# Optimization experiments

Hardware: AMD Instinct MI355X
Metric: run time of the kernel (lower is better)

The kernel has to match this reference:

```python
import jax, jax.numpy as jnp
import numpy as np

D_IN = 1024
D_OUT = 1024
N_HEADS = 16
HEAD_DIM = D_OUT // N_HEADS

def setup_inputs() -> dict:
    key = jax.random.key(0)
    ks = jax.random.split(key, 6)
    s = 0.02
    x = jax.random.normal(ks[0], (2, 2048, D_IN), dtype=jnp.float32)
    Wq = jax.random.normal(ks[1], (D_IN, D_OUT), dtype=jnp.float32) * s
    Wk = jax.random.normal(ks[2], (D_IN, D_OUT), dtype=jnp.float32) * s
    Wv = jax.random.normal(ks[3], (D_IN, D_OUT), dtype=jnp.float32) * s
    Wo = jax.random.normal(ks[4], (D_OUT, D_OUT), dtype=jnp.float32) * s
    bo = jnp.zeros((D_OUT,), dtype=jnp.float32)
    return {"x": x, "Wq": Wq, "Wk": Wk, "Wv": Wv, "Wo": Wo, "bo": bo}

def reference(x, Wq, Wk, Wv, Wo, bo):
    b, t, _ = x.shape
    # project and split heads: [b, h, t, d]
    def split_heads(y):
        return y.reshape(b, t, N_HEADS, HEAD_DIM).transpose(0, 2, 1, 3)
    q = split_heads(x @ Wq)
    k = split_heads(x @ Wk)
    v = split_heads(x @ Wv)
    # NOTE: original code applies NO 1/sqrt(head_dim) scaling
    scores = jnp.einsum('bhqd,bhkd->bhqk', q, k)
    causal = jnp.tril(jnp.ones((t, t), dtype=bool))  # keep lower triangle
    scores = jnp.where(causal, scores, -jnp.inf)
    attn = jax.nn.softmax(scores, axis=-1)
    ctx = jnp.einsum('bhqk,bhkd->bhqd', attn, v)
    ctx = ctx.transpose(0, 2, 1, 3).reshape(b, t, D_OUT)
    return ctx @ Wo + bo
```

## Files before the change

### kernel.cpp

```cpp
#include <hip/hip_runtime.h>

typedef unsigned short u16;
typedef unsigned int   u32;
typedef __bf16 bf16x2 __attribute__((ext_vector_type(2)));
typedef __bf16 bf16x8 __attribute__((ext_vector_type(8)));
typedef float  f32x4  __attribute__((ext_vector_type(4)));
typedef float  f32x16 __attribute__((ext_vector_type(16)));
typedef u32    u32x4  __attribute__((ext_vector_type(4)));

#define LOG2E 1.4426950408889634f

__device__ __forceinline__ u16 f2bf(float f) {
  union { float f; u32 u; } v; v.f = f;
  u32 r = v.u + 0x7fffu + ((v.u >> 16) & 1u);
  return (u16)(r >> 16);
}

__device__ __forceinline__ u32 pack2(float lo, float hi) {
  bf16x2 p = { (__bf16)lo, (__bf16)hi };
  return __builtin_bit_cast(u32, p);
}

#define GLOAD_LDS16(g, s) __builtin_amdgcn_global_load_lds( \
    (const __attribute__((address_space(1))) void*)(g),     \
    (__attribute__((address_space(3))) void*)(s), 16, 0, 0)


__global__ void k_convert(const float* __restrict__ in, u16* __restrict__ out) {
  int i = (blockIdx.x * 256 + threadIdx.x) * 8;
  float4 a = *(const float4*)(in + i);
  float4 b = *(const float4*)(in + i + 4);
  u16 o[8] = { f2bf(a.x), f2bf(a.y), f2bf(a.z), f2bf(a.w),
               f2bf(b.x), f2bf(b.y), f2bf(b.z), f2bf(b.w) };
  *(uint4*)(out + i) = *(const uint4*)o;
}

__global__ void k_transpose_w4(const float* __restrict__ Wq, const float* __restrict__ Wk,
                               const float* __restrict__ Wv, const float* __restrict__ Wo,
                               u16* __restrict__ WqkvT, u16* __restrict__ WoT) {
  const int z = blockIdx.z;
  const float* W = (z == 0) ? Wq : (z == 1) ? Wk : (z == 2) ? Wv : Wo;
  u16* WT = (z < 3) ? (WqkvT + ((size_t)z << 20)) : WoT;
  __shared__ float tile[64][65];
  const int t = threadIdx.x;
  const int n0 = blockIdx.x * 64, k0 = blockIdx.y * 64;
  const int r = t >> 4, c4 = (t & 15) * 4;
  #pragma unroll
  for (int rr = 0; rr < 64; rr += 16) {
    float4 v = *(const float4*)(W + (size_t)(k0 + r + rr) * 1024 + n0 + c4);
    tile[r + rr][c4]     = v.x; tile[r + rr][c4 + 1] = v.y;
    tile[r + rr][c4 + 2] = v.z; tile[r + rr][c4 + 3] = v.w;
  }
  __syncthreads();
  #pragma unroll
  for (int rr = 0; rr < 64; rr += 16) {
    u16 o[4] = { f2bf(tile[c4][r + rr]),     f2bf(tile[c4 + 1][r + rr]),
                 f2bf(tile[c4 + 2][r + rr]), f2bf(tile[c4 + 3][r + rr]) };
    *(ushort4*)(WT + (size_t)(n0 + r + rr) * 1024 + k0 + c4) = *(const ushort4*)o;
  }
}


template<int MODE>
__global__ __launch_bounds__(256) void k_gemm_bt(
    const u16* __restrict__ A, const u16* __restrict__ BT,
    void* __restrict__ Cv, const float* __restrict__ bias,
    int M, int N, int K) {
  __shared__ u16 lA[2][128 * 32];
  __shared__ u16 lB[2][128 * 32];
  const int t = threadIdx.x;
  const int l = t & 63, w = t >> 6;
  const int bM = blockIdx.y * 128, bN = blockIdx.x * 128;
  const int wr = w >> 1, wc = w & 1;
  const int NT = K >> 5;

  f32x4 acc[4][4] = {};

  const int fA  = w * 512 + l * 8;
  const int r0  = fA >> 5;
  const int kc0 = fA & 31;

  auto stage = [&](int buf, int kt) {
    const u16* ga = A  + (size_t)(bM + r0) * K + kt * 32 + kc0;
    const u16* gb = BT + (size_t)(bN + r0) * K + kt * 32 + kc0;
    GLOAD_LDS16(ga, &lA[buf][w * 512]);
    GLOAD_LDS16(gb, &lB[buf][w * 512]);
    GLOAD_LDS16(ga + (size_t)64 * K, &lA[buf][2048 + w * 512]);
    GLOAD_LDS16(gb + (size_t)64 * K, &lB[buf][2048 + w * 512]);
  };

  stage(0, 0);
  __syncthreads();
  int buf = 0;
  for (int kt = 0; kt < NT; ++kt) {
    if (kt + 1 < NT) stage(buf ^ 1, kt + 1);
    bf16x8 af[4], bfr[4];
    #pragma unroll
    for (int m = 0; m < 4; ++m)
      af[m] = *(const bf16x8*)&lA[buf][(wr * 64 + m * 16 + (l & 15)) * 32 + (l >> 4) * 8];
    #pragma unroll
    for (int n = 0; n < 4; ++n)
      bfr[n] = *(const bf16x8*)&lB[buf][(wc * 64 + n * 16 + (l & 15)) * 32 + (l >> 4) * 8];
    #pragma unroll
    for (int m = 0; m < 4; ++m)
      #pragma unroll
      for (int n = 0; n < 4; ++n)
        acc[m][n] = __builtin_amdgcn_mfma_f32_16x16x32_bf16(af[m], bfr[n], acc[m][n], 0, 0, 0);
    __syncthreads();
    buf ^= 1;
  }

  #pragma unroll
  for (int m = 0; m < 4; ++m) {
    #pragma unroll
    for (int n = 0; n < 4; ++n) {
      const int row = bM + wr * 64 + m * 16 + (l >> 4) * 4;
      const int col = bN + wc * 64 + n * 16 + (l & 15);
      if (MODE == 1) {
        #pragma unroll
        for (int i = 0; i < 4; ++i)
          ((float*)Cv)[(size_t)(row + i) * N + col] = acc[m][n][i] + bias[col];
      } else if (MODE == 0) {
        #pragma unroll
        for (int i = 0; i < 4; ++i)
          ((u16*)Cv)[(size_t)(row + i) * N + col] = f2bf(acc[m][n][i]);
      } else {
        const int which = col >> 10;
        const int h  = (col >> 6) & 15;
        const int d  = col & 63;
        const int bh = (row >> 11) * 16 + h;
        const int tile = (row & 2047) >> 5;
        const int tk = row & 31;
        u16* base = (u16*)Cv + (size_t)which * 4194304 + (size_t)bh * 131072 + tile * 2048;
        if (which == 2) {
          const int chunk = (d >> 5) * 2 + ((tk >> 4) & 1);
          const int lane  = (d & 31) + ((tk >> 3) & 1) * 32;
          const int j     = tk & 7;
          u16 o[4] = { f2bf(acc[m][n][0]), f2bf(acc[m][n][1]),
                       f2bf(acc[m][n][2]), f2bf(acc[m][n][3]) };
          *(ushort4*)(base + chunk * 512 + lane * 8 + j) = *(const ushort4*)o;
        } else {
          const float qs = (which == 0) ? LOG2E : 1.0f;
          const int chunk = d >> 4;
          const int j     = d & 7;
          const int lane0 = tk + ((d >> 3) & 1) * 32;
          #pragma unroll
          for (int i = 0; i < 4; ++i)
            base[chunk * 512 + (lane0 + i) * 8 + j] = f2bf(acc[m][n][i] * qs);
        }
      }
    }
  }
}


__global__ __launch_bounds__(256, 4) void k_attn(
    const u16* __restrict__ qt_, const u16* __restrict__ kt_,
    const u16* __restrict__ vt_, u16* __restrict__ ctx) {
  __shared__ float obuf[4][32][64];
  __shared__ float lbuf[4][32];
  __shared__ float rbuf[32];

  const int t = threadIdx.x;
  const int l = t & 63, w = t >> 6;
  const int hi = l >> 5, ln = l & 31;
  const int bidx = blockIdx.x;
  const int x = bidx & 7;
  const int bh = x * 4 + ((bidx >> 3) & 3);
  const int j = bidx >> 5;
  const int bb = bh >> 4, h = bh & 15;
  const size_t tokbase = (size_t)bb * 2048;
  const size_t hplane = (size_t)bh * 131072;

  const int B  = 64 - j;
  const int s0 = (65 * w) >> 2, s1 = (65 * (w + 1)) >> 2;
  const int l8 = l * 8;

  f32x16 oa = {}, ob = {};
  float lh = 0.f;

  auto process = [&](const u16* kb, const u16* vb, const bf16x8 (&qf)[4], bool diag) {
    bf16x8 kf[4];
    #pragma unroll
    for (int ds = 0; ds < 4; ++ds)
      kf[ds] = *(const bf16x8*)(kb + ds * 512 + l8);

    f32x16 sc = {};
    #pragma unroll
    for (int ds = 0; ds < 4; ++ds)
      sc = __builtin_amdgcn_mfma_f32_32x32x16_bf16(kf[ds], qf[ds], sc, 0, 0, 0);

    bf16x8 v00 = *(const bf16x8*)(vb + l8);
    bf16x8 v01 = *(const bf16x8*)(vb + 512 + l8);
    bf16x8 v10 = *(const bf16x8*)(vb + 1024 + l8);
    bf16x8 v11 = *(const bf16x8*)(vb + 1536 + l8);

    if (diag) {
      #pragma unroll
      for (int r = 0; r < 16; ++r) {
        const int kloc = (r & 3) + 8 * (r >> 2) + 4 * hi;
        if (kloc > ln) sc[r] = -__builtin_inff();
      }
    }

    float ph[16];
    #pragma unroll
    for (int r = 0; r < 16; ++r) ph[r] = exp2f(sc[r]);
    float b0 = ph[0] + ph[1],   b1 = ph[2] + ph[3];
    float b2 = ph[4] + ph[5],   b3 = ph[6] + ph[7];
    float b4 = ph[8] + ph[9],   b5 = ph[10] + ph[11];
    float b6 = ph[12] + ph[13], b7 = ph[14] + ph[15];
    lh += ((b0 + b1) + (b2 + b3)) + ((b4 + b5) + (b6 + b7));

    u32 c0 = pack2(ph[0],  ph[1]),  c1 = pack2(ph[2],  ph[3]);
    u32 c2 = pack2(ph[4],  ph[5]),  c3 = pack2(ph[6],  ph[7]);
    u32 c4 = pack2(ph[8],  ph[9]),  c5 = pack2(ph[10], ph[11]);
    u32 c6 = pack2(ph[12], ph[13]), c7 = pack2(ph[14], ph[15]);
    asm volatile("v_permlane32_swap_b32 %0, %1" : "+v"(c0), "+v"(c2));
    asm volatile("v_permlane32_swap_b32 %0, %1" : "+v"(c1), "+v"(c3));
    asm volatile("v_permlane32_swap_b32 %0, %1" : "+v"(c4), "+v"(c6));
    asm volatile("v_permlane32_swap_b32 %0, %1" : "+v"(c5), "+v"(c7));
    u32x4 wa0 = { c0, c1, c2, c3 };
    u32x4 wa1 = { c4, c5, c6, c7 };
    bf16x8 pa0 = __builtin_bit_cast(bf16x8, wa0);
    bf16x8 pa1 = __builtin_bit_cast(bf16x8, wa1);

    oa = __builtin_amdgcn_mfma_f32_32x32x16_bf16(pa0, v00, oa, 0, 0, 0);
    oa = __builtin_amdgcn_mfma_f32_32x32x16_bf16(pa1, v01, oa, 0, 0, 0);
    ob = __builtin_amdgcn_mfma_f32_32x32x16_bf16(pa0, v10, ob, 0, 0, 0);
    ob = __builtin_amdgcn_mfma_f32_32x32x16_bf16(pa1, v11, ob, 0, 0, 0);
  };

  auto stash = [&](int slot) {
    const float lr = lh + __shfl_xor(lh, 32);
    if (hi == 0) lbuf[slot][ln] = lr;
    #pragma unroll
    for (int r = 0; r < 16; ++r) {
      const int rm = (r & 3) + 8 * (r >> 2) + 4 * hi;
      obuf[slot][rm][ln]      = oa[r];
      obuf[slot][rm][ln + 32] = ob[r];
    }
  };

  auto runChain = [&](int qt, int k0, int k1) {
    if (k0 >= k1) return;
    bf16x8 qf[4];
    const u16* qq = qt_ + hplane + qt * 2048 + l8;
    #pragma unroll
    for (int ds = 0; ds < 4; ++ds) qf[ds] = *(const bf16x8*)(qq + ds * 512);
    const u16* kb = kt_ + hplane + k0 * 2048;
    const u16* vb = vt_ + hplane + k0 * 2048;
    for (int kt = k0; kt < k1; ++kt) {
      process(kb, vb, qf, kt == qt);
      kb += 2048; vb += 2048;
    }
  };

  auto mergeWrite = [&](int qt) {
    if (t < 32) {
      const int q = t;
      rbuf[q] = 1.0f / (lbuf[0][q] + lbuf[1][q] + lbuf[2][q] + lbuf[3][q]);
    }
    __syncthreads();
    u16* cb = ctx + (tokbase + qt * 32) * 1024 + h * 64;
    #pragma unroll
    for (int k2 = 0; k2 < 8; ++k2) {
      const int idx = t + k2 * 256;
      const int q = idx >> 6, d = idx & 63;
      const float v = obuf[0][q][d] + obuf[1][q][d] + obuf[2][q][d] + obuf[3][q][d];
      cb[(size_t)q * 1024 + d] = f2bf(v * rbuf[q]);
    }
  };

  runChain(63 - j, s0, (s1 < B) ? s1 : B);
  stash(w);
  oa = f32x16{}; ob = f32x16{}; lh = 0.f;
  runChain(j, ((s0 > B) ? s0 : B) - B, s1 - B);

  __syncthreads();
  mergeWrite(63 - j);
  __syncthreads();
  stash(w);
  __syncthreads();
  mergeWrite(j);
}


extern "C" void kernel_launch(void* const* d_in, const int* in_sizes, int n_in,
                              void* d_out, int out_size, void* d_ws, size_t ws_size,
                              hipStream_t stream) {
  const float* x  = (const float*)d_in[0];
  const float* Wq = (const float*)d_in[1];
  const float* Wk = (const float*)d_in[2];
  const float* Wv = (const float*)d_in[3];
  const float* Wo = (const float*)d_in[4];
  const float* bo = (const float*)d_in[5];
  float* out = (float*)d_out;
  char* ws = (char*)d_ws;

  u16* xb    = (u16*)(ws);
  u16* WqkvT = (u16*)(ws + (8u  << 20));
  u16* WoT   = (u16*)(ws + (14u << 20));
  u16* Qt    = (u16*)(ws + (16u << 20));
  u16* Kt    = (u16*)(ws + (24u << 20));
  u16* Vt    = (u16*)(ws + (32u << 20));
  u16* ctxb  = (u16*)(ws + (40u << 20));

  k_convert<<<2048, 256, 0, stream>>>(x, xb);
  k_transpose_w4<<<dim3(16, 16, 4), 256, 0, stream>>>(Wq, Wk, Wv, Wo, WqkvT, WoT);

  k_gemm_bt<2><<<dim3(24, 32), 256, 0, stream>>>(xb, WqkvT, Qt, nullptr, 4096, 3072, 1024);
  k_attn<<<1024, 256, 0, stream>>>(Qt, Kt, Vt, ctxb);
  k_gemm_bt<1><<<dim3(8, 32), 256, 0, stream>>>(ctxb, WoT, out, bo, 4096, 1024, 1024);
}
```

Baseline: 106.9 us.

## Add dedicated 256x256-tile QKV GEMM kernel with phased LDS prefetch

Replaces the generic 128x128 QKV projection GEMM with a dedicated kernel. It uses 512 threads, 256x256 output tiles, and a double-buffered LDS pipeline. Direct global-to-LDS loads are issued per phase, interleaved with MFMA work, and guarded by explicit vmcnt waits and s_setprio. The aim is more data reuse per tile and better overlap of memory and compute. The trade-off is fewer blocks (192 instead of 768) and higher register and LDS pressure.

```diff
diff --git a/kernel.cpp b/kernel.cpp
--- a/kernel.cpp
+++ b/kernel.cpp
@@ -120,34 +120,100 @@
         #pragma unroll
         for (int i = 0; i < 4; ++i)
           ((float*)Cv)[(size_t)(row + i) * N + col] = acc[m][n][i] + bias[col];
-      } else if (MODE == 0) {
+      } else {
         #pragma unroll
         for (int i = 0; i < 4; ++i)
           ((u16*)Cv)[(size_t)(row + i) * N + col] = f2bf(acc[m][n][i]);
+      }
+    }
+  }
+}
+
+
+__global__ __launch_bounds__(512) void k_gemm_qkv(
+    const u16* __restrict__ A, const u16* __restrict__ BT,
+    u16* __restrict__ Cv) {
+  __shared__ u16 L[2][4][8192];
+  const int t = threadIdx.x;
+  const int l = t & 63, w = t >> 6;
+  const int wr = w >> 2, wc = w & 3;
+  const int bM = blockIdx.y * 256, bN = blockIdx.x * 256;
+  const int K = 1024;
+
+  f32x4 acc[8][4] = {};
+
+  const int rlo = l & 15;
+  const int kof = (l >> 4) * 8;
+
+  auto stageReg = [&](int nb, int r, int kt) {
+    const int kh = r >> 1;
+    const int kk = kt * 64 + kh * 32 + kof;
+    const u16* m0 = (r & 1) ? (BT + (size_t)(bN + w * 16 + rlo) * K + kk)
+                            : (A  + (size_t)(bM + w * 16 + rlo) * K + kk);
+    const u16* m1 = m0 + (size_t)128 * K;
+    GLOAD_LDS16(m0, &L[nb][r][w * 512]);
+    GLOAD_LDS16(m1, &L[nb][r][w * 512 + 4096]);
+  };
+
+  stageReg(0, 0, 0); stageReg(0, 1, 0); stageReg(0, 2, 0); stageReg(0, 3, 0);
+
+  const int l8 = l * 8;
+  for (int kt = 0; kt < 16; ++kt) {
+    const int cur = kt & 1, nb = cur ^ 1;
+    const int sk = (kt + 1 < 16) ? kt + 1 : 15;
+    #pragma unroll
+    for (int ph = 0; ph < 4; ++ph) {
+      const int ks = ph >> 1, mh = ph & 1;
+      if ((ph & 1) == 0) asm volatile("s_waitcnt vmcnt(4)" ::: "memory");
+      __builtin_amdgcn_s_barrier();
+      bf16x8 af[4], bf[4];
+      #pragma unroll
+      for (int mi = 0; mi < 4; ++mi)
+        af[mi] = *(const bf16x8*)&L[cur][ks * 2][(wr * 8 + mh * 4 + mi) * 512 + l8];
+      #pragma unroll
+      for (int ni = 0; ni < 4; ++ni)
+        bf[ni] = *(const bf16x8*)&L[cur][ks * 2 + 1][(wc * 4 + ni) * 512 + l8];
+      stageReg(nb, ph, sk);
+      __builtin_amdgcn_s_setprio(1);
+      #pragma unroll
+      for (int mi = 0; mi < 4; ++mi)
+        #pragma unroll
+        for (int ni = 0; ni < 4; ++ni)
+          acc[mh * 4 + mi][ni] = __builtin_amdgcn_mfma_f32_16x16x32_bf16(
+              af[mi], bf[ni], acc[mh * 4 + mi][ni], 0, 0, 0);
+      __builtin_amdgcn_s_setprio(0);
+    }
+  }
+  asm volatile("s_waitcnt vmcnt(0)" ::: "memory");
+
+  #pragma unroll
+  for (int mi8 = 0; mi8 < 8; ++mi8) {
+    #pragma unroll
+    for (int ni = 0; ni < 4; ++ni) {
+      const int row = bM + wr * 128 + mi8 * 16 + (l >> 4) * 4;
+      const int col = bN + wc * 64 + ni * 16 + (l & 15);
+      const int which = col >> 10;
+      const int h  = (col >> 6) & 15;
+      const int d  = col & 63;
+      const int bh = (row >> 11) * 16 + h;
+      const int tile = (row & 2047) >> 5;
+      const int tk = row & 31;
+      u16* base = Cv + (size_t)which * 4194304 + (size_t)bh * 131072 + tile * 2048;
+      if (which == 2) {
+        const int chunk = (d >> 5) * 2 + ((tk >> 4) & 1);
+        const int lane  = (d & 31) + ((tk >> 3) & 1) * 32;
+        const int jj    = tk & 7;
+        u16 o[4] = { f2bf(acc[mi8][ni][0]), f2bf(acc[mi8][ni][1]),
+                     f2bf(acc[mi8][ni][2]), f2bf(acc[mi8][ni][3]) };
+        *(ushort4*)(base + chunk * 512 + lane * 8 + jj) = *(const ushort4*)o;
       } else {
-        const int which = col >> 10;
-        const int h  = (col >> 6) & 15;
-        const int d  = col & 63;
-        const int bh = (row >> 11) * 16 + h;
-        const int tile = (row & 2047) >> 5;
-        const int tk = row & 31;
-        u16* base = (u16*)Cv + (size_t)which * 4194304 + (size_t)bh * 131072 + tile * 2048;
-        if (which == 2) {
-          const int chunk = (d >> 5) * 2 + ((tk >> 4) & 1);
-          const int lane  = (d & 31) + ((tk >> 3) & 1) * 32;
-          const int j     = tk & 7;
-          u16 o[4] = { f2bf(acc[m][n][0]), f2bf(acc[m][n][1]),
-                       f2bf(acc[m][n][2]), f2bf(acc[m][n][3]) };
-          *(ushort4*)(base + chunk * 512 + lane * 8 + j) = *(const ushort4*)o;
-        } else {
-          const float qs = (which == 0) ? LOG2E : 1.0f;
-          const int chunk = d >> 4;
-          const int j     = d & 7;
-          const int lane0 = tk + ((d >> 3) & 1) * 32;
-          #pragma unroll
-          for (int i = 0; i < 4; ++i)
-            base[chunk * 512 + (lane0 + i) * 8 + j] = f2bf(acc[m][n][i] * qs);
-        }
+        const float qs = (which == 0) ? LOG2E : 1.0f;
+        const int chunk = d >> 4;
+        const int jj    = d & 7;
+        const int lane0 = tk + ((d >> 3) & 1) * 32;
+        #pragma unroll
+        for (int i = 0; i < 4; ++i)
+          base[chunk * 512 + (lane0 + i) * 8 + jj] = f2bf(acc[mi8][ni][i] * qs);
       }
     }
   }
@@ -309,7 +375,7 @@
   k_convert<<<2048, 256, 0, stream>>>(x, xb);
   k_transpose_w4<<<dim3(16, 16, 4), 256, 0, stream>>>(Wq, Wk, Wv, Wo, WqkvT, WoT);
 
-  k_gemm_bt<2><<<dim3(24, 32), 256, 0, stream>>>(xb, WqkvT, Qt, nullptr, 4096, 3072, 1024);
+  k_gemm_qkv<<<dim3(12, 16), 512, 0, stream>>>(xb, WqkvT, Qt);
   k_attn<<<1024, 256, 0, stream>>>(Qt, Kt, Vt, ctxb);
   k_gemm_bt<1><<<dim3(8, 32), 256, 0, stream>>>(ctxb, WoT, out, bo, 4096, 1024, 1024);
 }
```

New measurement: 110.8 us. 1.04x slower.
